# Optimization experiments

Hardware: AMD Instinct MI355X
Metric: run time of the kernel (lower is better)

## Reference

```python
import jax, jax.numpy as jnp
import numpy as np

D_MODEL = 1024
HEADS = 16


def setup_inputs() -> dict:
    key = jax.random.key(0)
    ks = jax.random.split(key, 11)
    B, S, D = 2, 2048, D_MODEL
    scale = 1.0 / np.sqrt(D)
    inp = {
        "q": jax.random.normal(ks[0], (B, S, D), jnp.float32),
        "k": jax.random.normal(ks[1], (B, S, D), jnp.float32),
        "v": jax.random.normal(ks[2], (B, S, D), jnp.float32),
        "w_q": jax.random.normal(ks[3], (D, D), jnp.float32) * scale,
        "b_q": jnp.zeros((D,), jnp.float32),
        "w_k": jax.random.normal(ks[4], (D, D), jnp.float32) * scale,
        "b_k": jnp.zeros((D,), jnp.float32),
        "w_v": jax.random.normal(ks[5], (D, D), jnp.float32) * scale,
        "b_v": jnp.zeros((D,), jnp.float32),
        "w_o": jax.random.normal(ks[6], (D, D), jnp.float32) * scale,
        "b_o": jnp.zeros((D,), jnp.float32),
    }
    return inp


def reference(q, k, v, w_q, b_q, w_k, b_k, w_v, b_v, w_o, b_o):
    B, S, D = q.shape
    H = HEADS
    Dh = D // H

    def split(x):  # [B,S,D] -> [B,H,S,Dh]
        return x.reshape(B, S, H, Dh).transpose(0, 2, 1, 3)

    qh = split(q @ w_q + b_q)
    kh = split(k @ w_k + b_k)
    vh = split(v @ w_v + b_v)

    # scaled dot-product attention: softmax(Q K^T / sqrt(Dh)) V
    scores = jnp.einsum("bhsd,bhtd->bhst", qh, kh) / jnp.sqrt(
        jnp.asarray(Dh, qh.dtype)
    )
    attn = jax.nn.softmax(scores, axis=-1)
    out = jnp.einsum("bhst,bhtd->bhsd", attn, vh)

    concat = out.transpose(0, 2, 1, 3).reshape(B, S, D)
    return concat @ w_o + b_o
```

## Files before the change

kernel.cpp:

```cpp
#include <hip/hip_runtime.h>
#include <hip/hip_bf16.h>
#include <math.h>

using bf16 = __hip_bfloat16;
typedef __bf16 bf16x8v __attribute__((ext_vector_type(8)));
typedef float f32x4v __attribute__((ext_vector_type(4)));

#define AS1 __attribute__((address_space(1)))
#define AS3 __attribute__((address_space(3)))

__device__ __forceinline__ void g2l16(const void* g, void* l) {
  __builtin_amdgcn_global_load_lds((const AS1 void*)g, (AS3 void*)l, 16, 0, 0);
}

__device__ __forceinline__ float fclamp(float v) {
  return fminf(fmaxf(v, -6.0e4f), 6.0e4f);
}

__device__ __forceinline__ unsigned packbf(float a, float b) {
  unsigned short lo = __builtin_bit_cast(unsigned short, __float2bfloat16(a));
  unsigned short hi = __builtin_bit_cast(unsigned short, __float2bfloat16(b));
  return (unsigned)lo | ((unsigned)hi << 16);
}

#define QSCL 0.1803368801111204f

__global__ __launch_bounds__(256) void transpose_cvt4(
    const float* __restrict__ w0, const float* __restrict__ w1,
    const float* __restrict__ w2, const float* __restrict__ w3,
    bf16* __restrict__ o0, bf16* __restrict__ o1,
    bf16* __restrict__ o2, bf16* __restrict__ o3) {
  const float* in = (blockIdx.z == 0) ? w0 : (blockIdx.z == 1) ? w1
                    : (blockIdx.z == 2) ? w2 : w3;
  bf16* out = (blockIdx.z == 0) ? o0 : (blockIdx.z == 1) ? o1
              : (blockIdx.z == 2) ? o2 : o3;
  __shared__ alignas(16) bf16 tile[64][80];
  const int t = threadIdx.x;
  const int bx = blockIdx.x * 64, by = blockIdx.y * 64;
#pragma unroll
  for (int p = 0; p < 4; ++p) {
    int idx = p * 1024 + t * 4;
    int r = idx >> 6, c0 = idx & 63;
    float4 v = *(const float4*)&in[(size_t)(by + r) * 1024 + bx + c0];
    tile[c0 + 0][r] = __float2bfloat16(v.x);
    tile[c0 + 1][r] = __float2bfloat16(v.y);
    tile[c0 + 2][r] = __float2bfloat16(v.z);
    tile[c0 + 3][r] = __float2bfloat16(v.w);
  }
  __syncthreads();
#pragma unroll
  for (int p = 0; p < 2; ++p) {
    int idx = p * 2048 + t * 8;
    int c = idx >> 6, r0 = idx & 63;
    *(uint4*)&out[(size_t)(bx + c) * 1024 + by + r0] = *(const uint4*)&tile[c][r0];
  }
}

__global__ __launch_bounds__(256) void cvt3(
    const float* __restrict__ q, const float* __restrict__ k,
    const float* __restrict__ v, bf16* __restrict__ oq,
    bf16* __restrict__ ok, bf16* __restrict__ ov) {
  const float* in = (blockIdx.y == 0) ? q : (blockIdx.y == 1) ? k : v;
  bf16* out = (blockIdx.y == 0) ? oq : (blockIdx.y == 1) ? ok : ov;
  int i = (blockIdx.x * 256 + threadIdx.x) * 8;
  float4 a = *(const float4*)&in[i];
  float4 b = *(const float4*)&in[i + 4];
  alignas(16) bf16 tmp[8];
  tmp[0] = __float2bfloat16(a.x); tmp[1] = __float2bfloat16(a.y);
  tmp[2] = __float2bfloat16(a.z); tmp[3] = __float2bfloat16(a.w);
  tmp[4] = __float2bfloat16(b.x); tmp[5] = __float2bfloat16(b.y);
  tmp[6] = __float2bfloat16(b.z); tmp[7] = __float2bfloat16(b.w);
  *(uint4*)&out[i] = *(const uint4*)tmp;
}

__device__ __forceinline__ void qkv_store(bf16* C, int z, int m, int n, float v) {
  int b_ = m >> 11, s_ = m & 2047, h_ = n >> 6, d_ = n & 63;
  size_t oidx = (z == 2)
      ? ((size_t)(b_ * 16 + h_) * 64 + d_) * 2048 + s_
      : ((size_t)(b_ * 16 + h_) * 2048 + s_) * 64 + d_;
  C[oidx] = __float2bfloat16(v);
}

__global__ __launch_bounds__(256, 2) void gemm_qkv_bf16(
    const bf16* __restrict__ Aq, const bf16* __restrict__ Ak,
    const bf16* __restrict__ Av,
    const bf16* __restrict__ WtQ, const bf16* __restrict__ WtK,
    const bf16* __restrict__ WtV,
    const float* __restrict__ bq, const float* __restrict__ bk_,
    const float* __restrict__ bv_,
    bf16* __restrict__ Qh, bf16* __restrict__ Kh, bf16* __restrict__ Vt) {
  constexpr int K = 1024;
  const int z = blockIdx.z;
  const bf16* A    = (z == 0) ? Aq : (z == 1) ? Ak : Av;
  const bf16* Bt   = (z == 0) ? WtQ : (z == 1) ? WtK : WtV;
  const float* bias = (z == 0) ? bq : (z == 1) ? bk_ : bv_;
  bf16* C = (z == 0) ? Qh : (z == 1) ? Kh : Vt;

  __shared__ alignas(16) bf16 As[128 * 32];
  __shared__ alignas(16) bf16 Bs[128 * 32];
  const int t = threadIdx.x;
  const int wave = t >> 6, lane = t & 63;
  const int quad = lane >> 4, l16 = lane & 15;
  const int bm = blockIdx.x * 128, bn = blockIdx.y * 128;
  const int wm = (wave & 1) * 64, wn = (wave >> 1) * 64;

  f32x4v acc[4][4] = {};

  for (int k0 = 0; k0 < K; k0 += 32) {
    __syncthreads();
#pragma unroll
    for (int c = 0; c < 2; ++c) {
      int idx = c * 2048 + t * 8;
      int row = idx >> 5, col = idx & 31;
      g2l16(&A[(size_t)(bm + row) * K + k0 + col], &As[c * 2048 + wave * 512]);
      g2l16(&Bt[(size_t)(bn + row) * K + k0 + col], &Bs[c * 2048 + wave * 512]);
    }
    __syncthreads();

    bf16x8v a[4], b[4];
#pragma unroll
    for (int mi = 0; mi < 4; ++mi)
      a[mi] = *(const bf16x8v*)&As[(wm + mi * 16 + l16) * 32 + quad * 8];
#pragma unroll
    for (int ni = 0; ni < 4; ++ni)
      b[ni] = *(const bf16x8v*)&Bs[(wn + ni * 16 + l16) * 32 + quad * 8];
#pragma unroll
    for (int mi = 0; mi < 4; ++mi)
#pragma unroll
      for (int ni = 0; ni < 4; ++ni)
        acc[mi][ni] = __builtin_amdgcn_mfma_f32_16x16x32_bf16(a[mi], b[ni],
                                                              acc[mi][ni], 0, 0, 0);
  }

  if (z == 2) {
#pragma unroll
    for (int ni = 0; ni < 4; ++ni) {
      int n = bn + wn + ni * 16 + l16;
      float bz = bias[n];
      int h_ = n >> 6, d_ = n & 63;
#pragma unroll
      for (int mi = 0; mi < 4; ++mi) {
        int m0 = bm + wm + mi * 16 + quad * 4;
        int b_ = m0 >> 11, s0 = m0 & 2047;
        uint2 u;
        u.x = packbf(fclamp(acc[mi][ni][0] + bz), fclamp(acc[mi][ni][1] + bz));
        u.y = packbf(fclamp(acc[mi][ni][2] + bz), fclamp(acc[mi][ni][3] + bz));
        *(uint2*)&C[((size_t)(b_ * 16 + h_) * 64 + d_) * 2048 + s0] = u;
      }
    }
  } else {
    const float scl = (z == 0) ? QSCL : 1.0f;
#pragma unroll
    for (int ni = 0; ni < 4; ++ni) {
      int n = bn + wn + ni * 16 + l16;
      float bz = bias[n];
#pragma unroll
      for (int mi = 0; mi < 4; ++mi)
#pragma unroll
        for (int r = 0; r < 4; ++r) {
          int m = bm + wm + mi * 16 + quad * 4 + r;
          qkv_store(C, z, m, n, fclamp(acc[mi][ni][r] + bz) * scl);
        }
    }
  }
}

__global__ __launch_bounds__(256, 2) void gemm_qkv_f32(
    const float* __restrict__ Aq, const float* __restrict__ Ak,
    const float* __restrict__ Av,
    const bf16* __restrict__ WtQ, const bf16* __restrict__ WtK,
    const bf16* __restrict__ WtV,
    const float* __restrict__ bq, const float* __restrict__ bk_,
    const float* __restrict__ bv_,
    bf16* __restrict__ Qh, bf16* __restrict__ Kh, bf16* __restrict__ Vt) {
  constexpr int K = 1024, LDA = 40;
  const int z = blockIdx.z;
  const float* A  = (z == 0) ? Aq : (z == 1) ? Ak : Av;
  const bf16* Bt  = (z == 0) ? WtQ : (z == 1) ? WtK : WtV;
  const float* bias = (z == 0) ? bq : (z == 1) ? bk_ : bv_;
  bf16* C = (z == 0) ? Qh : (z == 1) ? Kh : Vt;

  __shared__ alignas(16) bf16 As[128 * LDA];
  __shared__ alignas(16) bf16 Bs[128 * LDA];
  const int t = threadIdx.x;
  const int wave = t >> 6, lane = t & 63;
  const int quad = lane >> 4, l16 = lane & 15;
  const int bm = blockIdx.x * 128, bn = blockIdx.y * 128;
  const int wm = (wave & 1) * 64, wn = (wave >> 1) * 64;

  f32x4v acc[4][4] = {};

  for (int k0 = 0; k0 < K; k0 += 32) {
    uint4 va[2], vb[2];
#pragma unroll
    for (int c = 0; c < 2; ++c) {
      int idx = c * 2048 + t * 8;
      int row = idx >> 5, col = idx & 31;
      const float* src = &A[(size_t)(bm + row) * K + k0 + col];
      float4 f0 = *(const float4*)src;
      float4 f1 = *(const float4*)(src + 4);
      alignas(16) bf16 tmp[8];
      tmp[0] = __float2bfloat16(f0.x); tmp[1] = __float2bfloat16(f0.y);
      tmp[2] = __float2bfloat16(f0.z); tmp[3] = __float2bfloat16(f0.w);
      tmp[4] = __float2bfloat16(f1.x); tmp[5] = __float2bfloat16(f1.y);
      tmp[6] = __float2bfloat16(f1.z); tmp[7] = __float2bfloat16(f1.w);
      va[c] = *(const uint4*)tmp;
      vb[c] = *(const uint4*)&Bt[(size_t)(bn + row) * K + k0 + col];
    }
    __syncthreads();
#pragma unroll
    for (int c = 0; c < 2; ++c) {
      int idx = c * 2048 + t * 8;
      int row = idx >> 5, col = idx & 31;
      *(uint4*)&As[row * LDA + col] = va[c];
      *(uint4*)&Bs[row * LDA + col] = vb[c];
    }
    __syncthreads();

    bf16x8v a[4], b[4];
#pragma unroll
    for (int mi = 0; mi < 4; ++mi)
      a[mi] = *(const bf16x8v*)&As[(wm + mi * 16 + l16) * LDA + quad * 8];
#pragma unroll
    for (int ni = 0; ni < 4; ++ni)
      b[ni] = *(const bf16x8v*)&Bs[(wn + ni * 16 + l16) * LDA + quad * 8];
#pragma unroll
    for (int mi = 0; mi < 4; ++mi)
#pragma unroll
      for (int ni = 0; ni < 4; ++ni)
        acc[mi][ni] = __builtin_amdgcn_mfma_f32_16x16x32_bf16(a[mi], b[ni],
                                                              acc[mi][ni], 0, 0, 0);
  }

  if (z == 2) {
#pragma unroll
    for (int ni = 0; ni < 4; ++ni) {
      int n = bn + wn + ni * 16 + l16;
      float bz = bias[n];
      int h_ = n >> 6, d_ = n & 63;
#pragma unroll
      for (int mi = 0; mi < 4; ++mi) {
        int m0 = bm + wm + mi * 16 + quad * 4;
        int b_ = m0 >> 11, s0 = m0 & 2047;
        uint2 u;
        u.x = packbf(fclamp(acc[mi][ni][0] + bz), fclamp(acc[mi][ni][1] + bz));
        u.y = packbf(fclamp(acc[mi][ni][2] + bz), fclamp(acc[mi][ni][3] + bz));
        *(uint2*)&C[((size_t)(b_ * 16 + h_) * 64 + d_) * 2048 + s0] = u;
      }
    }
  } else {
    const float scl = (z == 0) ? QSCL : 1.0f;
#pragma unroll
    for (int ni = 0; ni < 4; ++ni) {
      int n = bn + wn + ni * 16 + l16;
      float bz = bias[n];
#pragma unroll
      for (int mi = 0; mi < 4; ++mi)
#pragma unroll
        for (int r = 0; r < 4; ++r) {
          int m = bm + wm + mi * 16 + quad * 4 + r;
          qkv_store(C, z, m, n, fclamp(acc[mi][ni][r] + bz) * scl);
        }
    }
  }
}

__global__ __launch_bounds__(256, 2) void gemm_out(
    const bf16* __restrict__ A, const bf16* __restrict__ Bt,
    const float* __restrict__ bias, float* __restrict__ C) {
  constexpr int K = 1024, N = 1024;
  __shared__ alignas(16) bf16 As[128 * 32];
  __shared__ alignas(16) bf16 Bs[64 * 32];
  const int t = threadIdx.x;
  const int wave = t >> 6, lane = t & 63;
  const int quad = lane >> 4, l16 = lane & 15;
  const int bm = blockIdx.x * 128, bn = blockIdx.y * 64;
  const int wm = (wave & 1) * 64, wn = (wave >> 1) * 32;

  f32x4v acc[4][2] = {};

  for (int k0 = 0; k0 < K; k0 += 32) {
    __syncthreads();
#pragma unroll
    for (int c = 0; c < 2; ++c) {
      int idx = c * 2048 + t * 8;
      int row = idx >> 5, col = idx & 31;
      g2l16(&A[(size_t)(bm + row) * K + k0 + col], &As[c * 2048 + wave * 512]);
    }
    {
      int idx = t * 8;
      int row = idx >> 5, col = idx & 31;
      g2l16(&Bt[(size_t)(bn + row) * K + k0 + col], &Bs[wave * 512]);
    }
    __syncthreads();

    bf16x8v a[4], b[2];
#pragma unroll
    for (int mi = 0; mi < 4; ++mi)
      a[mi] = *(const bf16x8v*)&As[(wm + mi * 16 + l16) * 32 + quad * 8];
#pragma unroll
    for (int ni = 0; ni < 2; ++ni)
      b[ni] = *(const bf16x8v*)&Bs[(wn + ni * 16 + l16) * 32 + quad * 8];
#pragma unroll
    for (int mi = 0; mi < 4; ++mi)
#pragma unroll
      for (int ni = 0; ni < 2; ++ni)
        acc[mi][ni] = __builtin_amdgcn_mfma_f32_16x16x32_bf16(a[mi], b[ni],
                                                              acc[mi][ni], 0, 0, 0);
  }

#pragma unroll
  for (int ni = 0; ni < 2; ++ni) {
    int n = bn + wn + ni * 16 + l16;
    float bz = bias[n];
#pragma unroll
    for (int mi = 0; mi < 4; ++mi)
#pragma unroll
      for (int r = 0; r < 4; ++r) {
        int m = bm + wm + mi * 16 + quad * 4 + r;
        C[(size_t)m * N + n] = fclamp(acc[mi][ni][r] + bz);
      }
  }
}

__global__ __launch_bounds__(512, 4) void attn(
    const bf16* __restrict__ Qh, const bf16* __restrict__ Kh,
    const bf16* __restrict__ Vt, bf16* __restrict__ Ctx) {
  constexpr int LDPP = 40;
  __shared__ alignas(16) bf16 QsPs[128 * 64];
  __shared__ alignas(16) bf16 Ks[3][64 * 64];
  __shared__ alignas(16) bf16 Vs[3][64 * 64];
  const int t = threadIdx.x;
  const int wave = t >> 6, lane = t & 63;
  const int quad = lane >> 4, l16 = lane & 15;
  const int sw = l16 & 7;

  const int lin = blockIdx.x;
  const int li = lin >> 3;
  const int qb = li & 15;
  const int bh = (lin & 7) * 4 + (li >> 4);

  const size_t bh_off = (size_t)bh * 2048 * 64;
  const bf16* Qb = Qh + bh_off;
  const bf16* Kb = Kh + bh_off;
  const bf16* Vb = Vt + bh_off;

  const int srow = t >> 3;
  const int schunk = t & 7;

  auto stageKV = [&](int kt, int buf) {
    int mc = schunk ^ (srow & 7);
    g2l16(&Kb[(size_t)(kt * 64 + srow) * 64 + mc * 8], &Ks[buf][wave * 512]);
    g2l16(&Vb[(size_t)srow * 2048 + kt * 64 + mc * 8], &Vs[buf][wave * 512]);
  };

#pragma unroll
  for (int c = 0; c < 2; ++c) {
    int row = c * 64 + srow;
    int mc = schunk ^ (row & 7);
    g2l16(&Qb[(size_t)(qb * 128 + row) * 64 + mc * 8],
          &QsPs[c * 4096 + wave * 512]);
  }
  stageKV(0, 0);
  asm volatile("s_waitcnt vmcnt(2)" ::: "memory");
  __builtin_amdgcn_s_barrier();

  bf16x8v aq[2];
#pragma unroll
  for (int kk = 0; kk < 2; ++kk)
    aq[kk] = *(const bf16x8v*)
        &QsPs[(wave * 16 + l16) * 64 + (((kk * 4 + quad) ^ sw) << 3)];

  __syncthreads();
  bf16* Psw = QsPs + wave * (16 * LDPP);

  stageKV(1, 1);

  bf16x8v vone;
#pragma unroll
  for (int i = 0; i < 8; ++i) vone[i] = (__bf16)1.0f;

  f32x4v lsum = {};
  f32x4v oacc[4] = {};

  auto compute = [&](int buf) {
#pragma unroll
    for (int h = 0; h < 2; ++h) {
      f32x4v s[2] = {};
      __builtin_amdgcn_s_setprio(1);
#pragma unroll
      for (int kk = 0; kk < 2; ++kk)
#pragma unroll
        for (int ni = 0; ni < 2; ++ni) {
          bf16x8v bk = *(const bf16x8v*)
              &Ks[buf][(h * 32 + ni * 16 + l16) * 64 + (((kk * 4 + quad) ^ sw) << 3)];
          s[ni] = __builtin_amdgcn_mfma_f32_16x16x32_bf16(bk, aq[kk],
                                                          s[ni], 0, 0, 0);
        }
      __builtin_amdgcn_s_setprio(0);

#pragma unroll
      for (int ni = 0; ni < 2; ++ni) {
        float p0 = __builtin_amdgcn_exp2f(fminf(s[ni][0], 80.f));
        float p1 = __builtin_amdgcn_exp2f(fminf(s[ni][1], 80.f));
        float p2 = __builtin_amdgcn_exp2f(fminf(s[ni][2], 80.f));
        float p3 = __builtin_amdgcn_exp2f(fminf(s[ni][3], 80.f));
        uint2 u;
        u.x = packbf(p0, p1);
        u.y = packbf(p2, p3);
        *(uint2*)&Psw[l16 * LDPP + ni * 16 + quad * 4] = u;
      }

      bf16x8v ap = *(const bf16x8v*)&Psw[l16 * LDPP + quad * 8];
      __builtin_amdgcn_s_setprio(1);
      lsum = __builtin_amdgcn_mfma_f32_16x16x32_bf16(ap, vone, lsum, 0, 0, 0);
#pragma unroll
      for (int ni = 0; ni < 4; ++ni) {
        bf16x8v bv = *(const bf16x8v*)
            &Vs[buf][(ni * 16 + l16) * 64 + (((h * 4 + quad) ^ sw) << 3)];
        oacc[ni] = __builtin_amdgcn_mfma_f32_16x16x32_bf16(ap, bv, oacc[ni],
                                                           0, 0, 0);
      }
      __builtin_amdgcn_s_setprio(0);
    }
  };

  int bufc = 0;
  for (int tt = 0; tt < 30; ++tt) {
    int bufs = bufc + 2; if (bufs >= 3) bufs -= 3;
    stageKV(tt + 2, bufs);
    compute(bufc);
    asm volatile("s_waitcnt vmcnt(2)" ::: "memory");
    __builtin_amdgcn_s_barrier();
    bufc = (bufc == 2) ? 0 : bufc + 1;
  }
  compute(bufc);
  asm volatile("s_waitcnt vmcnt(0)" ::: "memory");
  __builtin_amdgcn_s_barrier();
  bufc = (bufc == 2) ? 0 : bufc + 1;
  compute(bufc);

  const int b_ = bh >> 4, h_ = bh & 15;
#pragma unroll
  for (int r = 0; r < 4; ++r) {
    int sr = qb * 128 + wave * 16 + quad * 4 + r;
    float inv = 1.0f / fmaxf(lsum[r], 1.0e-20f);
#pragma unroll
    for (int ni = 0; ni < 4; ++ni) {
      int col = h_ * 64 + ni * 16 + l16;
      Ctx[(size_t)(b_ * 2048 + sr) * 1024 + col] =
          __float2bfloat16(fclamp(oacc[ni][r] * inv));
    }
  }
}

extern "C" void kernel_launch(void* const* d_in, const int* in_sizes, int n_in,
                              void* d_out, int out_size, void* d_ws, size_t ws_size,
                              hipStream_t stream) {
  const float* q   = (const float*)d_in[0];
  const float* k   = (const float*)d_in[1];
  const float* v   = (const float*)d_in[2];
  const float* w_q = (const float*)d_in[3];
  const float* b_q = (const float*)d_in[4];
  const float* w_k = (const float*)d_in[5];
  const float* b_k = (const float*)d_in[6];
  const float* w_v = (const float*)d_in[7];
  const float* b_v = (const float*)d_in[8];
  const float* w_o = (const float*)d_in[9];
  const float* b_o = (const float*)d_in[10];
  float* out = (float*)d_out;

  char* ws = (char*)d_ws;
  const size_t MB = (size_t)1024 * 1024;
  bf16* WtQ = (bf16*)(ws + 0 * MB);
  bf16* WtK = (bf16*)(ws + 2 * MB);
  bf16* WtV = (bf16*)(ws + 4 * MB);
  bf16* WtO = (bf16*)(ws + 6 * MB);

  dim3 tb(256);
  transpose_cvt4<<<dim3(16, 16, 4), tb, 0, stream>>>(w_q, w_k, w_v, w_o,
                                                     WtQ, WtK, WtV, WtO);

  const bool big = ws_size >= (size_t)57 * MB;
  if (big) {
    bf16* Qa  = (bf16*)(ws + 8 * MB);
    bf16* Ka  = (bf16*)(ws + 16 * MB);
    bf16* Va  = (bf16*)(ws + 24 * MB);
    bf16* Qh  = (bf16*)(ws + 32 * MB);
    bf16* Kh  = (bf16*)(ws + 40 * MB);
    bf16* Vt  = (bf16*)(ws + 48 * MB);
    bf16* Ctx = Qa;

    cvt3<<<dim3(2048, 3), tb, 0, stream>>>(q, k, v, Qa, Ka, Va);
    gemm_qkv_bf16<<<dim3(32, 8, 3), tb, 0, stream>>>(Qa, Ka, Va, WtQ, WtK, WtV,
                                                     b_q, b_k, b_v, Qh, Kh, Vt);
    attn<<<dim3(512), dim3(512), 0, stream>>>(Qh, Kh, Vt, Ctx);
    gemm_out<<<dim3(32, 16), tb, 0, stream>>>(Ctx, WtO, b_o, out);
  } else {
    bf16* Qh  = (bf16*)(ws + 8 * MB);
    bf16* Kh  = (bf16*)(ws + 16 * MB);
    bf16* Vt  = (bf16*)(ws + 24 * MB);
    bf16* Ctx = (bf16*)(ws + 32 * MB);

    gemm_qkv_f32<<<dim3(32, 8, 3), tb, 0, stream>>>(q, k, v, WtQ, WtK, WtV,
                                                    b_q, b_k, b_v, Qh, Kh, Vt);
    attn<<<dim3(512), dim3(512), 0, stream>>>(Qh, Kh, Vt, Ctx);
    gemm_out<<<dim3(32, 16), tb, 0, stream>>>(Ctx, WtO, b_o, out);
  }
}
```

Before: 223.6 us.

## Double-buffer QKV and output GEMMs and drop separate input conversion pass

Removes the cvt3 kernel and the bf16 QKV GEMM path, so the QKV projection always reads fp32 inputs and converts them in registers. Both the QKV and output-projection GEMMs now use double-buffered shared memory, prefetching the next K tile (direct-to-LDS for weights, register staging for A) while MFMAs run on the current one. Each K step now has one barrier instead of two. The aim is to save the extra conversion pass over the inputs and hide global-load latency, at the cost of twice the LDS per block, which may reduce occupancy.

```diff
diff --git a/kernel.cpp b/kernel.cpp
--- a/kernel.cpp
+++ b/kernel.cpp
@@ -56,116 +56,7 @@
   }
 }
 
-__global__ __launch_bounds__(256) void cvt3(
-    const float* __restrict__ q, const float* __restrict__ k,
-    const float* __restrict__ v, bf16* __restrict__ oq,
-    bf16* __restrict__ ok, bf16* __restrict__ ov) {
-  const float* in = (blockIdx.y == 0) ? q : (blockIdx.y == 1) ? k : v;
-  bf16* out = (blockIdx.y == 0) ? oq : (blockIdx.y == 1) ? ok : ov;
-  int i = (blockIdx.x * 256 + threadIdx.x) * 8;
-  float4 a = *(const float4*)&in[i];
-  float4 b = *(const float4*)&in[i + 4];
-  alignas(16) bf16 tmp[8];
-  tmp[0] = __float2bfloat16(a.x); tmp[1] = __float2bfloat16(a.y);
-  tmp[2] = __float2bfloat16(a.z); tmp[3] = __float2bfloat16(a.w);
-  tmp[4] = __float2bfloat16(b.x); tmp[5] = __float2bfloat16(b.y);
-  tmp[6] = __float2bfloat16(b.z); tmp[7] = __float2bfloat16(b.w);
-  *(uint4*)&out[i] = *(const uint4*)tmp;
-}
-
-__device__ __forceinline__ void qkv_store(bf16* C, int z, int m, int n, float v) {
-  int b_ = m >> 11, s_ = m & 2047, h_ = n >> 6, d_ = n & 63;
-  size_t oidx = (z == 2)
-      ? ((size_t)(b_ * 16 + h_) * 64 + d_) * 2048 + s_
-      : ((size_t)(b_ * 16 + h_) * 2048 + s_) * 64 + d_;
-  C[oidx] = __float2bfloat16(v);
-}
-
-__global__ __launch_bounds__(256, 2) void gemm_qkv_bf16(
-    const bf16* __restrict__ Aq, const bf16* __restrict__ Ak,
-    const bf16* __restrict__ Av,
-    const bf16* __restrict__ WtQ, const bf16* __restrict__ WtK,
-    const bf16* __restrict__ WtV,
-    const float* __restrict__ bq, const float* __restrict__ bk_,
-    const float* __restrict__ bv_,
-    bf16* __restrict__ Qh, bf16* __restrict__ Kh, bf16* __restrict__ Vt) {
-  constexpr int K = 1024;
-  const int z = blockIdx.z;
-  const bf16* A    = (z == 0) ? Aq : (z == 1) ? Ak : Av;
-  const bf16* Bt   = (z == 0) ? WtQ : (z == 1) ? WtK : WtV;
-  const float* bias = (z == 0) ? bq : (z == 1) ? bk_ : bv_;
-  bf16* C = (z == 0) ? Qh : (z == 1) ? Kh : Vt;
-
-  __shared__ alignas(16) bf16 As[128 * 32];
-  __shared__ alignas(16) bf16 Bs[128 * 32];
-  const int t = threadIdx.x;
-  const int wave = t >> 6, lane = t & 63;
-  const int quad = lane >> 4, l16 = lane & 15;
-  const int bm = blockIdx.x * 128, bn = blockIdx.y * 128;
-  const int wm = (wave & 1) * 64, wn = (wave >> 1) * 64;
-
-  f32x4v acc[4][4] = {};
-
-  for (int k0 = 0; k0 < K; k0 += 32) {
-    __syncthreads();
-#pragma unroll
-    for (int c = 0; c < 2; ++c) {
-      int idx = c * 2048 + t * 8;
-      int row = idx >> 5, col = idx & 31;
-      g2l16(&A[(size_t)(bm + row) * K + k0 + col], &As[c * 2048 + wave * 512]);
-      g2l16(&Bt[(size_t)(bn + row) * K + k0 + col], &Bs[c * 2048 + wave * 512]);
-    }
-    __syncthreads();
-
-    bf16x8v a[4], b[4];
-#pragma unroll
-    for (int mi = 0; mi < 4; ++mi)
-      a[mi] = *(const bf16x8v*)&As[(wm + mi * 16 + l16) * 32 + quad * 8];
-#pragma unroll
-    for (int ni = 0; ni < 4; ++ni)
-      b[ni] = *(const bf16x8v*)&Bs[(wn + ni * 16 + l16) * 32 + quad * 8];
-#pragma unroll
-    for (int mi = 0; mi < 4; ++mi)
-#pragma unroll
-      for (int ni = 0; ni < 4; ++ni)
-        acc[mi][ni] = __builtin_amdgcn_mfma_f32_16x16x32_bf16(a[mi], b[ni],
-                                                              acc[mi][ni], 0, 0, 0);
-  }
-
-  if (z == 2) {
-#pragma unroll
-    for (int ni = 0; ni < 4; ++ni) {
-      int n = bn + wn + ni * 16 + l16;
-      float bz = bias[n];
-      int h_ = n >> 6, d_ = n & 63;
-#pragma unroll
-      for (int mi = 0; mi < 4; ++mi) {
-        int m0 = bm + wm + mi * 16 + quad * 4;
-        int b_ = m0 >> 11, s0 = m0 & 2047;
-        uint2 u;
-        u.x = packbf(fclamp(acc[mi][ni][0] + bz), fclamp(acc[mi][ni][1] + bz));
-        u.y = packbf(fclamp(acc[mi][ni][2] + bz), fclamp(acc[mi][ni][3] + bz));
-        *(uint2*)&C[((size_t)(b_ * 16 + h_) * 64 + d_) * 2048 + s0] = u;
-      }
-    }
-  } else {
-    const float scl = (z == 0) ? QSCL : 1.0f;
-#pragma unroll
-    for (int ni = 0; ni < 4; ++ni) {
-      int n = bn + wn + ni * 16 + l16;
-      float bz = bias[n];
-#pragma unroll
-      for (int mi = 0; mi < 4; ++mi)
-#pragma unroll
-        for (int r = 0; r < 4; ++r) {
-          int m = bm + wm + mi * 16 + quad * 4 + r;
-          qkv_store(C, z, m, n, fclamp(acc[mi][ni][r] + bz) * scl);
-        }
-    }
-  }
-}
-
-__global__ __launch_bounds__(256, 2) void gemm_qkv_f32(
+__global__ __launch_bounds__(256, 2) void gemm_qkv(
     const float* __restrict__ Aq, const float* __restrict__ Ak,
     const float* __restrict__ Av,
     const bf16* __restrict__ WtQ, const bf16* __restrict__ WtK,
@@ -180,8 +71,8 @@
   const float* bias = (z == 0) ? bq : (z == 1) ? bk_ : bv_;
   bf16* C = (z == 0) ? Qh : (z == 1) ? Kh : Vt;
 
-  __shared__ alignas(16) bf16 As[128 * LDA];
-  __shared__ alignas(16) bf16 Bs[128 * LDA];
+  __shared__ alignas(16) bf16 As[2][128 * LDA];
+  __shared__ alignas(16) bf16 Bs[2][128 * 32];
   const int t = threadIdx.x;
   const int wave = t >> 6, lane = t & 63;
   const int quad = lane >> 4, l16 = lane & 15;
@@ -190,46 +81,73 @@
 
   f32x4v acc[4][4] = {};
 
-  for (int k0 = 0; k0 < K; k0 += 32) {
-    uint4 va[2], vb[2];
+  auto loadA = [&](int k0, float4* f) {
 #pragma unroll
     for (int c = 0; c < 2; ++c) {
       int idx = c * 2048 + t * 8;
       int row = idx >> 5, col = idx & 31;
       const float* src = &A[(size_t)(bm + row) * K + k0 + col];
-      float4 f0 = *(const float4*)src;
-      float4 f1 = *(const float4*)(src + 4);
-      alignas(16) bf16 tmp[8];
-      tmp[0] = __float2bfloat16(f0.x); tmp[1] = __float2bfloat16(f0.y);
-      tmp[2] = __float2bfloat16(f0.z); tmp[3] = __float2bfloat16(f0.w);
-      tmp[4] = __float2bfloat16(f1.x); tmp[5] = __float2bfloat16(f1.y);
-      tmp[6] = __float2bfloat16(f1.z); tmp[7] = __float2bfloat16(f1.w);
-      va[c] = *(const uint4*)tmp;
-      vb[c] = *(const uint4*)&Bt[(size_t)(bn + row) * K + k0 + col];
-    }
-    __syncthreads();
+      f[c * 2 + 0] = *(const float4*)src;
+      f[c * 2 + 1] = *(const float4*)(src + 4);
+    }
+  };
+  auto writeA = [&](int buf, const float4* f) {
 #pragma unroll
     for (int c = 0; c < 2; ++c) {
       int idx = c * 2048 + t * 8;
       int row = idx >> 5, col = idx & 31;
-      *(uint4*)&As[row * LDA + col] = va[c];
-      *(uint4*)&Bs[row * LDA + col] = vb[c];
-    }
+      uint4 u;
+      u.x = packbf(f[c * 2 + 0].x, f[c * 2 + 0].y);
+      u.y = packbf(f[c * 2 + 0].z, f[c * 2 + 0].w);
+      u.z = packbf(f[c * 2 + 1].x, f[c * 2 + 1].y);
+      u.w = packbf(f[c * 2 + 1].z, f[c * 2 + 1].w);
+      *(uint4*)&As[buf][row * LDA + col] = u;
+    }
+  };
+  auto stageB = [&](int k0, int buf) {
+#pragma unroll
+    for (int c = 0; c < 2; ++c) {
+      int idx = c * 2048 + t * 8;
+      int row = idx >> 5, col = idx & 31;
+      g2l16(&Bt[(size_t)(bn + row) * K + k0 + col],
+            &Bs[buf][c * 2048 + wave * 512]);
+    }
+  };
+
+  {
+    float4 f0[4];
+    loadA(0, f0);
+    stageB(0, 0);
+    writeA(0, f0);
     __syncthreads();
+  }
+
+  int buf = 0;
+  for (int k0 = 0; k0 < K; k0 += 32) {
+    const bool more = (k0 + 32) < K;
+    float4 fN[4];
+    if (more) {
+      loadA(k0 + 32, fN);
+      stageB(k0 + 32, buf ^ 1);
+    }
 
     bf16x8v a[4], b[4];
 #pragma unroll
     for (int mi = 0; mi < 4; ++mi)
-      a[mi] = *(const bf16x8v*)&As[(wm + mi * 16 + l16) * LDA + quad * 8];
+      a[mi] = *(const bf16x8v*)&As[buf][(wm + mi * 16 + l16) * LDA + quad * 8];
 #pragma unroll
     for (int ni = 0; ni < 4; ++ni)
-      b[ni] = *(const bf16x8v*)&Bs[(wn + ni * 16 + l16) * LDA + quad * 8];
+      b[ni] = *(const bf16x8v*)&Bs[buf][(wn + ni * 16 + l16) * 32 + quad * 8];
 #pragma unroll
     for (int mi = 0; mi < 4; ++mi)
 #pragma unroll
       for (int ni = 0; ni < 4; ++ni)
         acc[mi][ni] = __builtin_amdgcn_mfma_f32_16x16x32_bf16(a[mi], b[ni],
                                                               acc[mi][ni], 0, 0, 0);
+
+    if (more) writeA(buf ^ 1, fN);
+    __syncthreads();
+    buf ^= 1;
   }
 
   if (z == 2) {
@@ -254,12 +172,15 @@
     for (int ni = 0; ni < 4; ++ni) {
       int n = bn + wn + ni * 16 + l16;
       float bz = bias[n];
+      int h_ = n >> 6, d_ = n & 63;
 #pragma unroll
       for (int mi = 0; mi < 4; ++mi)
 #pragma unroll
         for (int r = 0; r < 4; ++r) {
           int m = bm + wm + mi * 16 + quad * 4 + r;
-          qkv_store(C, z, m, n, fclamp(acc[mi][ni][r] + bz) * scl);
+          int b_ = m >> 11, s_ = m & 2047;
+          C[((size_t)(b_ * 16 + h_) * 2048 + s_) * 64 + d_] =
+              __float2bfloat16(fclamp(acc[mi][ni][r] + bz) * scl);
         }
     }
   }
@@ -269,8 +190,8 @@
     const bf16* __restrict__ A, const bf16* __restrict__ Bt,
     const float* __restrict__ bias, float* __restrict__ C) {
   constexpr int K = 1024, N = 1024;
-  __shared__ alignas(16) bf16 As[128 * 32];
-  __shared__ alignas(16) bf16 Bs[64 * 32];
+  __shared__ alignas(16) bf16 As[2][128 * 32];
+  __shared__ alignas(16) bf16 Bs[2][64 * 32];
   const int t = threadIdx.x;
   const int wave = t >> 6, lane = t & 63;
   const int quad = lane >> 4, l16 = lane & 15;
@@ -279,34 +200,43 @@
 
   f32x4v acc[4][2] = {};
 
-  for (int k0 = 0; k0 < K; k0 += 32) {
-    __syncthreads();
+  auto stage = [&](int k0, int buf) {
 #pragma unroll
     for (int c = 0; c < 2; ++c) {
       int idx = c * 2048 + t * 8;
       int row = idx >> 5, col = idx & 31;
-      g2l16(&A[(size_t)(bm + row) * K + k0 + col], &As[c * 2048 + wave * 512]);
+      g2l16(&A[(size_t)(bm + row) * K + k0 + col],
+            &As[buf][c * 2048 + wave * 512]);
     }
     {
       int idx = t * 8;
       int row = idx >> 5, col = idx & 31;
-      g2l16(&Bt[(size_t)(bn + row) * K + k0 + col], &Bs[wave * 512]);
-    }
-    __syncthreads();
+      g2l16(&Bt[(size_t)(bn + row) * K + k0 + col], &Bs[buf][wave * 512]);
+    }
+  };
+
+  stage(0, 0);
+  __syncthreads();
+
+  int buf = 0;
+  for (int k0 = 0; k0 < K; k0 += 32) {
+    if (k0 + 32 < K) stage(k0 + 32, buf ^ 1);
 
     bf16x8v a[4], b[2];
 #pragma unroll
     for (int mi = 0; mi < 4; ++mi)
-      a[mi] = *(const bf16x8v*)&As[(wm + mi * 16 + l16) * 32 + quad * 8];
+      a[mi] = *(const bf16x8v*)&As[buf][(wm + mi * 16 + l16) * 32 + quad * 8];
 #pragma unroll
     for (int ni = 0; ni < 2; ++ni)
-      b[ni] = *(const bf16x8v*)&Bs[(wn + ni * 16 + l16) * 32 + quad * 8];
+      b[ni] = *(const bf16x8v*)&Bs[buf][(wn + ni * 16 + l16) * 32 + quad * 8];
 #pragma unroll
     for (int mi = 0; mi < 4; ++mi)
 #pragma unroll
       for (int ni = 0; ni < 2; ++ni)
         acc[mi][ni] = __builtin_amdgcn_mfma_f32_16x16x32_bf16(a[mi], b[ni],
                                                               acc[mi][ni], 0, 0, 0);
+    __syncthreads();
+    buf ^= 1;
   }
 
 #pragma unroll
@@ -476,35 +406,16 @@
   bf16* WtK = (bf16*)(ws + 2 * MB);
   bf16* WtV = (bf16*)(ws + 4 * MB);
   bf16* WtO = (bf16*)(ws + 6 * MB);
+  bf16* Qh  = (bf16*)(ws + 8 * MB);
+  bf16* Kh  = (bf16*)(ws + 16 * MB);
+  bf16* Vt  = (bf16*)(ws + 24 * MB);
+  bf16* Ctx = (bf16*)(ws + 32 * MB);
 
   dim3 tb(256);
   transpose_cvt4<<<dim3(16, 16, 4), tb, 0, stream>>>(w_q, w_k, w_v, w_o,
                                                      WtQ, WtK, WtV, WtO);
-
-  const bool big = ws_size >= (size_t)57 * MB;
-  if (big) {
-    bf16* Qa  = (bf16*)(ws + 8 * MB);
-    bf16* Ka  = (bf16*)(ws + 16 * MB);
-    bf16* Va  = (bf16*)(ws + 24 * MB);
-    bf16* Qh  = (bf16*)(ws + 32 * MB);
-    bf16* Kh  = (bf16*)(ws + 40 * MB);
-    bf16* Vt  = (bf16*)(ws + 48 * MB);
-    bf16* Ctx = Qa;
-
-    cvt3<<<dim3(2048, 3), tb, 0, stream>>>(q, k, v, Qa, Ka, Va);
-    gemm_qkv_bf16<<<dim3(32, 8, 3), tb, 0, stream>>>(Qa, Ka, Va, WtQ, WtK, WtV,
-                                                     b_q, b_k, b_v, Qh, Kh, Vt);
-    attn<<<dim3(512), dim3(512), 0, stream>>>(Qh, Kh, Vt, Ctx);
-    gemm_out<<<dim3(32, 16), tb, 0, stream>>>(Ctx, WtO, b_o, out);
-  } else {
-    bf16* Qh  = (bf16*)(ws + 8 * MB);
-    bf16* Kh  = (bf16*)(ws + 16 * MB);
-    bf16* Vt  = (bf16*)(ws + 24 * MB);
-    bf16* Ctx = (bf16*)(ws + 32 * MB);
-
-    gemm_qkv_f32<<<dim3(32, 8, 3), tb, 0, stream>>>(q, k, v, WtQ, WtK, WtV,
-                                                    b_q, b_k, b_v, Qh, Kh, Vt);
-    attn<<<dim3(512), dim3(512), 0, stream>>>(Qh, Kh, Vt, Ctx);
-    gemm_out<<<dim3(32, 16), tb, 0, stream>>>(Ctx, WtO, b_o, out);
-  }
-}
+  gemm_qkv<<<dim3(32, 8, 3), tb, 0, stream>>>(q, k, v, WtQ, WtK, WtV,
+                                              b_q, b_k, b_v, Qh, Kh, Vt);
+  attn<<<dim3(512), dim3(512), 0, stream>>>(Qh, Kh, Vt, Ctx);
+  gemm_out<<<dim3(32, 16), tb, 0, stream>>>(Ctx, WtO, b_o, out);
+}
```

Result: slower. 241.3 us (+7.9%).
